# Kernel optimization log

Hardware: AMD Instinct MI355X
Metric: run time of the kernel (lower is better)

Reference implementation:

```python
import jax, jax.numpy as jnp
import numpy as np

N = 16777216
C = 2
HARD_WEIGHT = 1.4  # weight for target == 0
EASY_WEIGHT = 1.0  # weight for target == 1


def setup_inputs() -> dict:
    key = jax.random.key(0)
    k1, k2, k3 = jax.random.split(key, 3)
    logits = jax.random.normal(k1, (N, C), dtype=jnp.float32)
    targets = jax.random.randint(k2, (N,), 0, 2, dtype=jnp.int64)
    text_keys = jax.random.randint(k3, (N,), 0, 1000, dtype=jnp.int64)
    return {"logits": logits, "targets": targets, "text_keys": text_keys}


def reference(logits, targets, text_keys):
    # per-sample cross entropy: -log_softmax(logits)[i, targets[i]]
    logp = jax.nn.log_softmax(logits, axis=-1)
    ce = -jnp.take_along_axis(logp, targets[:, None].astype(jnp.int32), axis=-1)[:, 0]
    # difficulty weighting: 1.0 if target==1 else 1.4 (targets are binary)
    w = jnp.where(targets == 1, EASY_WEIGHT, HARD_WEIGHT).astype(ce.dtype)
    return jnp.mean(ce * w)
```

## Files before the change

kernel.cpp:

```cpp
#include <hip/hip_runtime.h>
#include <hip/hip_bf16.h>


#define NTHR 256
#define ABLK 8192

typedef float v4f __attribute__((ext_vector_type(4)));
typedef int   v2i __attribute__((ext_vector_type(2)));

__global__ __launch_bounds__(NTHR) void dwl_main_kernel(
    const float* __restrict__ logits,
    const int* __restrict__ targets,
    float* __restrict__ partials)
{
    const v4f* lg4 = reinterpret_cast<const v4f*>(logits);
    const v2i* tg2 = reinterpret_cast<const v2i*>(targets);

    const int base = blockIdx.x * (4 * NTHR) + threadIdx.x;

    v4f f[4];
    v2i t[4];
    #pragma unroll
    for (int k = 0; k < 4; ++k) {
        const int i = base + k * NTHR;
        f[k] = __builtin_nontemporal_load(&lg4[i]);
        t[k] = __builtin_nontemporal_load(&tg2[i]);
    }

    float acc = 0.0f;
    #pragma unroll
    for (int k = 0; k < 4; ++k) {
        #pragma unroll
        for (int j = 0; j < 2; ++j) {
            const float l0 = f[k][2 * j];
            const float l1 = f[k][2 * j + 1];
            const bool one = (t[k][j] == 1);
            const float d  = one ? (l0 - l1) : (l1 - l0);
            const float ce = fmaxf(d, 0.0f) + __logf(1.0f + __expf(-fabsf(d)));
            acc += one ? ce : 1.4f * ce;
        }
    }

    #pragma unroll
    for (int off = 32; off > 0; off >>= 1)
        acc += __shfl_down(acc, off);

    __shared__ float smem[NTHR / 64];
    const int lane = threadIdx.x & 63;
    const int wave = threadIdx.x >> 6;
    if (lane == 0) smem[wave] = acc;
    __syncthreads();

    if (threadIdx.x == 0) {
        float s = 0.0f;
        #pragma unroll
        for (int wv = 0; wv < NTHR / 64; ++wv) s += smem[wv];
        partials[blockIdx.x] = s;
    }
}

__global__ __launch_bounds__(NTHR) void dwl_final_kernel(
    const float* __restrict__ partials,
    float* __restrict__ out,
    float invN)
{
    double acc = 0.0;
    for (int i = threadIdx.x; i < ABLK; i += NTHR)
        acc += (double)partials[i];

    #pragma unroll
    for (int off = 32; off > 0; off >>= 1)
        acc += __shfl_down(acc, off);

    __shared__ double smem[NTHR / 64];
    const int lane = threadIdx.x & 63;
    const int wave = threadIdx.x >> 6;
    if (lane == 0) smem[wave] = acc;
    __syncthreads();

    if (threadIdx.x == 0) {
        double s = 0.0;
        #pragma unroll
        for (int wv = 0; wv < NTHR / 64; ++wv) s += smem[wv];
        out[0] = (float)(s * (double)invN);
    }
}

extern "C" void kernel_launch(void* const* d_in, const int* in_sizes, int n_in,
                              void* d_out, int out_size, void* d_ws, size_t ws_size,
                              hipStream_t stream) {
    const float* logits  = (const float*)d_in[0];
    const int*   targets = (const int*)d_in[1];

    const int n = in_sizes[1];
    float* partials = (float*)d_ws;
    float* out      = (float*)d_out;

    dwl_main_kernel<<<ABLK, NTHR, 0, stream>>>(logits, targets, partials);
    dwl_final_kernel<<<1, NTHR, 0, stream>>>(partials, out, (float)(1.0 / (double)n));
}
```

Before: 246.6 us.

## Use grid-stride persistent blocks with software-pipelined register prefetch

The grid shrinks from 8192 one-shot blocks to 2048 blocks that each loop over four slabs. The next slab's logits and targets are loaded into registers while the current slab's cross-entropy is computed, so loads overlap with math. Fewer blocks also means fewer partials for the final reduce and less block launch overhead. The cost is double-buffered register pressure and a hardcoded element count, which only fits N divisible by the stride.

```diff
diff --git a/kernel.cpp b/kernel.cpp
--- a/kernel.cpp
+++ b/kernel.cpp
@@ -3,30 +3,12 @@
 
 
 #define NTHR 256
-#define ABLK 8192
+#define NBLK 2048
 
 typedef float v4f __attribute__((ext_vector_type(4)));
 typedef int   v2i __attribute__((ext_vector_type(2)));
 
-__global__ __launch_bounds__(NTHR) void dwl_main_kernel(
-    const float* __restrict__ logits,
-    const int* __restrict__ targets,
-    float* __restrict__ partials)
-{
-    const v4f* lg4 = reinterpret_cast<const v4f*>(logits);
-    const v2i* tg2 = reinterpret_cast<const v2i*>(targets);
-
-    const int base = blockIdx.x * (4 * NTHR) + threadIdx.x;
-
-    v4f f[4];
-    v2i t[4];
-    #pragma unroll
-    for (int k = 0; k < 4; ++k) {
-        const int i = base + k * NTHR;
-        f[k] = __builtin_nontemporal_load(&lg4[i]);
-        t[k] = __builtin_nontemporal_load(&tg2[i]);
-    }
-
+__device__ __forceinline__ float slab_ce(const v4f f[4], const v2i t[4]) {
     float acc = 0.0f;
     #pragma unroll
     for (int k = 0; k < 4; ++k) {
@@ -40,6 +22,44 @@
             acc += one ? ce : 1.4f * ce;
         }
     }
+    return acc;
+}
+
+__global__ __launch_bounds__(NTHR) void dwl_main_kernel(
+    const float* __restrict__ logits,
+    const int* __restrict__ targets,
+    float* __restrict__ partials)
+{
+    const v4f* lg4 = reinterpret_cast<const v4f*>(logits);
+    const v2i* tg2 = reinterpret_cast<const v2i*>(targets);
+
+    const int nPairs = 8388608;
+    const int stride = NBLK * 4 * NTHR;
+    int base = blockIdx.x * (4 * NTHR) + threadIdx.x;
+
+    float acc = 0.0f;
+
+    v4f f[4]; v2i t[4];
+    #pragma unroll
+    for (int k = 0; k < 4; ++k) {
+        const int i = base + k * NTHR;
+        f[k] = __builtin_nontemporal_load(&lg4[i]);
+        t[k] = __builtin_nontemporal_load(&tg2[i]);
+    }
+
+    for (base += stride; base + 3 * NTHR < nPairs; base += stride) {
+        v4f fn[4]; v2i tn[4];
+        #pragma unroll
+        for (int k = 0; k < 4; ++k) {
+            const int i = base + k * NTHR;
+            fn[k] = __builtin_nontemporal_load(&lg4[i]);
+            tn[k] = __builtin_nontemporal_load(&tg2[i]);
+        }
+        acc += slab_ce(f, t);
+        #pragma unroll
+        for (int k = 0; k < 4; ++k) { f[k] = fn[k]; t[k] = tn[k]; }
+    }
+    acc += slab_ce(f, t);
 
     #pragma unroll
     for (int off = 32; off > 0; off >>= 1)
@@ -65,7 +85,7 @@
     float invN)
 {
     double acc = 0.0;
-    for (int i = threadIdx.x; i < ABLK; i += NTHR)
+    for (int i = threadIdx.x; i < NBLK; i += NTHR)
         acc += (double)partials[i];
 
     #pragma unroll
@@ -96,6 +116,6 @@
     float* partials = (float*)d_ws;
     float* out      = (float*)d_out;
 
-    dwl_main_kernel<<<ABLK, NTHR, 0, stream>>>(logits, targets, partials);
+    dwl_main_kernel<<<NBLK, NTHR, 0, stream>>>(logits, targets, partials);
     dwl_final_kernel<<<1, NTHR, 0, stream>>>(partials, out, (float)(1.0 / (double)n));
 }
```

Result: no change. 243.0 us (-1.4%).
